# Performance work log

Measured on AMD Instinct MI355X. Metric: run time of the kernel, lower is better.

## Reference

```python
import jax, jax.numpy as jnp
import numpy as np

EPS = 1e-12
IMU_NOISE_DIAG = np.array([1e-07, 1e-07, 0.01, 0.001], dtype=np.float32)
INIT_COVAR_SQRT = np.array([0, 0, 0, 0, 0, 0, 0.01, 0.01, 0.01, 1e-4, 1e-4, 1e-4,
                            1e-08, 1e-08, 1e-08, 0.1, 0.1, 0.1], dtype=np.float32)
TRANS_SCALE = 5.4
TS2 = TRANS_SCALE * TRANS_SCALE
VIS_INIT_GUESS = 10.0 / TS2
VIS_BETA, VIS_GAMMA = 3.0, 1.0
IMU_BETA, IMU_GAMMA = 4.0, 1.0


def skew3(v):  # (..., 3) -> (..., 3, 3)
    x, y, z = v[..., 0], v[..., 1], v[..., 2]
    o = jnp.zeros_like(x)
    return jnp.stack([jnp.stack([o, -z, y], -1),
                      jnp.stack([z, o, -x], -1),
                      jnp.stack([-y, x, o], -1)], -2)


def exp_SO3(phi):  # (..., 3) -> (..., 3, 3) Rodrigues
    theta2 = jnp.sum(phi * phi, axis=-1)
    theta = jnp.sqrt(theta2)
    small = theta < 1e-8
    th = jnp.where(small, 1.0, theta)
    A = jnp.where(small, 1.0 - theta2 / 6.0, jnp.sin(th) / th)[..., None, None]
    B = jnp.where(small, 0.5 - theta2 / 24.0, (1.0 - jnp.cos(th)) / (th * th))[..., None, None]
    K = skew3(phi)
    return jnp.eye(3, dtype=phi.dtype) + A * K + B * (K @ K)


def force_symmetrical(M):
    Mu = jnp.triu(M)
    n = M.shape[-1]
    return Mu + jnp.swapaxes(Mu, -1, -2) * (1.0 - jnp.eye(n, dtype=M.dtype))


def proc_vis_covar(vis_std):
    # vis_covar_scale is all ones (par.vis_covar_scale = 1.0)
    scale = jnp.ones((6,), dtype=vis_std.dtype)
    diag = VIS_INIT_GUESS * (10.0 ** (VIS_BETA * jnp.tanh(VIS_GAMMA * vis_std)))
    diag = diag / scale[None, :]
    return jax.vmap(jnp.diag)(diag)  # (2B, 6, 6)


def get_imu_noise_covar(imu_noise_weight):
    # Linear(1,4,bias=False) applied to ones(1): just the weight column
    covar = 10.0 ** (IMU_BETA * jnp.tanh(IMU_GAMMA * imu_noise_weight[:, 0]))  # (4,)
    diag = jnp.repeat(jnp.asarray(IMU_NOISE_DIAG), 3) * jnp.repeat(covar, 3)   # (12,)
    return jnp.diag(diag)


def propagate(dts, wa_xyzs, R_ckbts, g_k, imu_noise_covar, P0):
    B = dts.shape[0]
    T = dts.shape[1]
    I3 = jnp.eye(3, dtype=dts.dtype)
    I18 = jnp.eye(18, dtype=dts.dtype)

    def step(P, inp):
        dt, gyro, accel, R = inp  # (B,), (B,3), (B,3), (B,3,3)
        Rt = jnp.swapaxes(R, -1, -2)
        w = gyro  # bw_k = 0
        Rg = jnp.einsum('bij,bj->bi', Rt, g_k)
        a = accel - Rg  # ba_k = 0
        F = jnp.zeros((B, 18, 18), dtype=dt.dtype)
        F = F.at[:, 0:3, 0:3].set(-skew3(w))
        F = F.at[:, 0:3, 12:15].set(-I3)
        F = F.at[:, 3:6, 6:9].set(I3)
        F = F.at[:, 6:9, 0:3].set(-jnp.einsum('bij,bjk->bik', R, skew3(Rg + a)))
        F = F.at[:, 6:9, 9:12].set(-I3)
        F = F.at[:, 6:9, 15:18].set(-R)
        G = jnp.zeros((B, 18, 12), dtype=dt.dtype)
        G = G.at[:, 0:3, 0:3].set(-I3)
        G = G.at[:, 6:9, 6:9].set(-R)
        G = G.at[:, 12:15, 3:6].set(I3)
        G = G.at[:, 15:18, 9:12].set(I3)
        dtb = dt[:, None, None]
        Phi = I18 + F * dtb + 0.5 * (F @ F) * (dtb * dtb)
        Phi = Phi.at[:, 0:3, 0:3].set(jnp.swapaxes(exp_SO3(dt[:, None] * w), -1, -2))
        PhiT = jnp.swapaxes(Phi, -1, -2)
        Q = (Phi @ G @ imu_noise_covar @ jnp.swapaxes(G, -1, -2) @ PhiT) * dtb
        P = force_symmetrical(Phi @ P @ PhiT + Q)
        return P, None

    xs = (jnp.swapaxes(dts, 0, 1),                       # (T, B)
          jnp.swapaxes(wa_xyzs[:, :T, :3], 0, 1),        # (T, B, 3)
          jnp.swapaxes(wa_xyzs[:, :T, 3:], 0, 1),        # (T, B, 3)
          jnp.swapaxes(R_ckbts[:, :T], 0, 1))            # (T, B, 3, 3)
    P, _ = jax.lax.scan(step, P0, xs)
    return P


def update(preimu_rot, preimu_trans, P, vis_rot, vis_trans, vis_covar, H0, H1, v_ck, g_ck):
    B = vis_rot.shape[0]
    residual = jnp.concatenate([vis_rot - preimu_rot, vis_trans - preimu_trans], axis=1)  # (B,6)
    I3 = jnp.eye(3, dtype=vis_rot.dtype)
    H = jnp.zeros((B, 6, 18), dtype=vis_rot.dtype)
    H = H.at[:, 0:3, 0:3].set(H0)
    H = H.at[:, 3:6, 0:3].set(H1)
    H = H.at[:, 3:6, 3:6].set(I3)
    Ht = jnp.swapaxes(H, -1, -2)
    S = H @ P @ Ht + vis_covar                 # (B,6,6)
    K = P @ Ht @ jnp.linalg.inv(S)             # (B,18,6)
    est = K @ residual[..., None]              # (B,18,1)
    phi_e, p_e = est[:, 0:3], est[:, 3:6]
    v_e, g_e = est[:, 6:9], est[:, 9:12]
    ekf_phi = preimu_rot + (H0 @ phi_e)[..., 0]
    ekf_t = preimu_trans + (H1 @ phi_e)[..., 0] + p_e[..., 0]
    return ekf_phi, ekf_t, v_ck + v_e[..., 0], g_ck + g_e[..., 0]


def setup_inputs() -> dict:
    key = jax.random.key(0)
    ks = jax.random.split(key, 16)
    B2 = 8192
    d = {
        'dts': jax.random.uniform(ks[0], (B2, 11), jnp.float32) * 0.01,
        'wa_xyzs': jax.random.normal(ks[1], (B2, 12, 6), jnp.float32),
        'R_ckbts': jax.random.normal(ks[2], (B2, 12, 3, 3), jnp.float32),
        'velocities': jax.random.normal(ks[3], (B2, 3), jnp.float32),
        'gravities': jax.random.normal(ks[4], (B2, 3), jnp.float32),
        'H0': jax.random.normal(ks[5], (B2, 3, 3), jnp.float32),
        'H1': jax.random.normal(ks[6], (B2, 3, 3), jnp.float32),
        'preimu_rot': jax.random.normal(ks[7], (B2, 3), jnp.float32),
        'preimu_trans': jax.random.normal(ks[8], (B2, 3), jnp.float32),
        'vis_rot': jax.random.normal(ks[9], (B2, 3), jnp.float32),
        'vis_trans': jax.random.normal(ks[10], (B2, 3), jnp.float32),
        'vis_rot_std': jax.random.uniform(ks[11], (B2, 3), jnp.float32),
        'vis_trans_std': jax.random.uniform(ks[12], (B2, 3), jnp.float32),
        'init_covar_diag_sqrt': jnp.asarray(INIT_COVAR_SQRT),
        'imu_noise_weight': jnp.zeros((4, 1), jnp.float32),  # train_imu_noise_covar=False -> zeroed
    }
    return d


def reference(dts, wa_xyzs, R_ckbts, velocities, gravities, H0, H1,
              preimu_rot, preimu_trans, vis_rot, vis_trans,
              vis_rot_std, vis_trans_std, init_covar_diag_sqrt, imu_noise_weight):
    B2 = dts.shape[0]
    vis_std = jnp.concatenate([vis_rot_std, vis_trans_std], axis=1)
    vis_covar = proc_vis_covar(vis_std)
    vis_trans = vis_trans * TRANS_SCALE
    imu_noise_covar = get_imu_noise_covar(imu_noise_weight)
    P0_diag = init_covar_diag_sqrt * init_covar_diag_sqrt + EPS
    P0 = jnp.broadcast_to(jnp.diag(P0_diag), (B2, 18, 18))
    P = propagate(dts, wa_xyzs, R_ckbts, gravities, imu_noise_covar, P0)
    ekf_phi, ekf_t, ekf_v, ekf_g = update(preimu_rot, preimu_trans, P,
                                          vis_rot, vis_trans, vis_covar,
                                          H0, H1, velocities, gravities)
    return jnp.concatenate([ekf_phi, ekf_t, ekf_v, ekf_g], axis=1)  # (2B, 12)
```

## Files before the change

kernel.cpp:

```cpp
#include <hip/hip_runtime.h>
#include <math.h>

#define TSTEPS 11
#define PPB 7
#define LPP 9
#define STRIDE 228
#define PHT_OFF 0
#define S6_OFF 144
#define Y_OFF 192
#define EST_OFF 200

__device__ __forceinline__ float sel3(int c, float a, float b, float d) {
    float t = (c == 1) ? b : a;
    return (c == 2) ? d : t;
}

__global__ void __launch_bounds__(64)
ekf_kernel(const float* __restrict__ dts, const float* __restrict__ wa,
           const float* __restrict__ Rc, const float* __restrict__ vel,
           const float* __restrict__ grav, const float* __restrict__ H0g,
           const float* __restrict__ H1g, const float* __restrict__ prot,
           const float* __restrict__ ptrans, const float* __restrict__ vrot,
           const float* __restrict__ vtrans, const float* __restrict__ vrstd,
           const float* __restrict__ vtstd, const float* __restrict__ icds,
           const float* __restrict__ inw, float* __restrict__ out, int B)
{
    __shared__ __align__(16) float lds[PPB * STRIDE];
    const int tid = threadIdx.x;
    const int praw = tid / LPP;
    const int r = tid - praw * LPP;
    const int p = (praw < PPB) ? praw : (PPB - 1);
    const int b0 = blockIdx.x * PPB + p;
    const bool valid = (praw < PPB) && (b0 < B);
    const int b = (b0 < B) ? b0 : (B - 1);
    float* L = lds + p * STRIDE;

    const float qcA = 1e-7f * exp10f(4.f * tanhf(inw[0]));
    const float qcB = 1e-7f * exp10f(4.f * tanhf(inw[1]));
    const float qcC = 1e-2f * exp10f(4.f * tanhf(inw[2]));
    const float qcD = 1e-3f * exp10f(4.f * tanhf(inw[3]));

    const float g0 = grav[(size_t)b*3+0], g1 = grav[(size_t)b*3+1], g2 = grav[(size_t)b*3+2];

    float np[18], npb[18];
#pragma unroll
    for (int k = 0; k < 18; ++k) { np[k] = 0.f; npb[k] = 0.f; }
    { const float d0 = icds[r];     np[r]      = d0*d0 + 1e-12f;
      const float d1 = icds[9 + r]; npb[9 + r] = d1*d1 + 1e-12f; }

    float dt, Rm[9], w0, w1, w2, ar0, ar1, ar2;
    {
        dt = dts[(size_t)b * TSTEPS];
        const size_t rb = (size_t)b * 108;
#pragma unroll
        for (int i = 0; i < 9; ++i) Rm[i] = Rc[rb + i];
        const float2* wp = (const float2*)(wa + (size_t)b * 72);
        const float2 wq0 = wp[0], wq1 = wp[1], wq2 = wp[2];
        w0 = wq0.x; w1 = wq0.y; w2 = wq1.x; ar0 = wq1.y; ar1 = wq2.x; ar2 = wq2.y;
    }

    for (int t = 0; t < TSTEPS; ++t) {
        float dtn = 0.f, Rn[9], wn0 = 0.f, wn1 = 0.f, wn2 = 0.f, an0 = 0.f, an1 = 0.f, an2 = 0.f;
#pragma unroll
        for (int i = 0; i < 9; ++i) Rn[i] = 0.f;
        if (t + 1 < TSTEPS) {
            dtn = dts[(size_t)b * TSTEPS + t + 1];
            const size_t rb = (size_t)b * 108 + (size_t)(t + 1) * 9;
#pragma unroll
            for (int i = 0; i < 9; ++i) Rn[i] = Rc[rb + i];
            const float2* wp = (const float2*)(wa + (size_t)b * 72 + (size_t)(t + 1) * 6);
            const float2 wq0 = wp[0], wq1 = wp[1], wq2 = wp[2];
            wn0 = wq0.x; wn1 = wq0.y; wn2 = wq1.x; an0 = wq1.y; an1 = wq2.x; an2 = wq2.y;
        }

        const float hdt2 = 0.5f * dt * dt;
        const float Rg0 = Rm[0]*g0 + Rm[3]*g1 + Rm[6]*g2;
        const float Rg1 = Rm[1]*g0 + Rm[4]*g1 + Rm[7]*g2;
        const float Rg2 = Rm[2]*g0 + Rm[5]*g1 + Rm[8]*g2;
        const float a0 = Rg0 + (ar0 - Rg0);
        const float a1 = Rg1 + (ar1 - Rg1);
        const float a2 = Rg2 + (ar2 - Rg2);

        const float p0 = dt*w0, p1 = dt*w1, p2 = dt*w2;
        const float th2 = p0*p0 + p1*p1 + p2*p2;
        const float th4 = th2 * th2;
        const float A  = 1.f - th2*(1.f/6.f)  + th4*(1.f/120.f);
        const float Bc = 0.5f - th2*(1.f/24.f) + th4*(1.f/720.f);
        float E[9];
        E[0] =  Bc*(p0*p0 - th2);  E[1] =  A*p2 + Bc*p0*p1;  E[2] = -A*p1 + Bc*p0*p2;
        E[3] = -A*p2 + Bc*p1*p0;   E[4] =  Bc*(p1*p1 - th2); E[5] =  A*p0 + Bc*p1*p2;
        E[6] =  A*p1 + Bc*p2*p0;   E[7] = -A*p0 + Bc*p2*p1;  E[8] =  Bc*(p2*p2 - th2);
        float N[9];
        N[0] = -(Rm[1]*a2 - Rm[2]*a1);  N[1] = -(Rm[2]*a0 - Rm[0]*a2);  N[2] = -(Rm[0]*a1 - Rm[1]*a0);
        N[3] = -(Rm[4]*a2 - Rm[5]*a1);  N[4] = -(Rm[5]*a0 - Rm[3]*a2);  N[5] = -(Rm[3]*a1 - Rm[4]*a0);
        N[6] = -(Rm[7]*a2 - Rm[8]*a1);  N[7] = -(Rm[8]*a0 - Rm[6]*a2);  N[8] = -(Rm[6]*a1 - Rm[7]*a0);
        float M2[9];
#pragma unroll
        for (int c = 0; c < 3; ++c) {
            const float n0 = N[c*3], n1 = N[c*3+1], n2 = N[c*3+2];
            M2[c*3+0] = dt*n0 - hdt2*(n1*w2 - n2*w1);
            M2[c*3+1] = dt*n1 - hdt2*(n2*w0 - n0*w2);
            M2[c*3+2] = dt*n2 - hdt2*(n0*w1 - n1*w0);
        }

        auto Smv = [&](const float v[18], float o[9]) {
            const float ev0 = E[0]*v[0] + E[1]*v[1] + E[2]*v[2];
            const float ev1 = E[3]*v[0] + E[4]*v[1] + E[5]*v[2];
            const float ev2 = E[6]*v[0] + E[7]*v[1] + E[8]*v[2];
            const float cx0 = w1*v[14] - w2*v[13];
            const float cx1 = w2*v[12] - w0*v[14];
            const float cx2 = w0*v[13] - w1*v[12];
            o[0] = ev0 - dt*v[12] + hdt2*cx0;
            o[1] = ev1 - dt*v[13] + hdt2*cx1;
            o[2] = ev2 - dt*v[14] + hdt2*cx2;
            const float nv0 = N[0]*v[0] + N[1]*v[1] + N[2]*v[2];
            const float nv1 = N[3]*v[0] + N[4]*v[1] + N[5]*v[2];
            const float nv2 = N[6]*v[0] + N[7]*v[1] + N[8]*v[2];
            const float rv0 = Rm[0]*v[15] + Rm[1]*v[16] + Rm[2]*v[17];
            const float rv1 = Rm[3]*v[15] + Rm[4]*v[16] + Rm[5]*v[17];
            const float rv2 = Rm[6]*v[15] + Rm[7]*v[16] + Rm[8]*v[17];
            o[3] = hdt2*nv0 + dt*v[6] - hdt2*v[9]  - hdt2*rv0;
            o[4] = hdt2*nv1 + dt*v[7] - hdt2*v[10] - hdt2*rv1;
            o[5] = hdt2*nv2 + dt*v[8] - hdt2*v[11] - hdt2*rv2;
            const float mv0 = M2[0]*v[0] + M2[1]*v[1] + M2[2]*v[2];
            const float mv1 = M2[3]*v[0] + M2[4]*v[1] + M2[5]*v[2];
            const float mv2 = M2[6]*v[0] + M2[7]*v[1] + M2[8]*v[2];
            const float nw0 = N[0]*v[12] + N[1]*v[13] + N[2]*v[14];
            const float nw1 = N[3]*v[12] + N[4]*v[13] + N[5]*v[14];
            const float nw2 = N[6]*v[12] + N[7]*v[13] + N[8]*v[14];
            o[6] = mv0 - dt*v[9]  - hdt2*nw0 - dt*rv0;
            o[7] = mv1 - dt*v[10] - hdt2*nw1 - dt*rv1;
            o[8] = mv2 - dt*v[11] - hdt2*nw2 - dt*rv2;
        };

        float uca[9], ucb[9];
        Smv(np, uca);
        Smv(npb, ucb);
#pragma unroll
        for (int i = 0; i < 9; ++i) {
            L[i*20 + r]     = uca[i];
            L[i*20 + 9 + r] = ucb[i];
        }
        __syncthreads();

        float ur[18];
        {
            const float4* up = (const float4*)&L[r*20];
            const float4 q0 = up[0], q1 = up[1], q2 = up[2], q3 = up[3];
            const float2 q4 = *(const float2*)&L[r*20 + 16];
            ur[0]=q0.x; ur[1]=q0.y; ur[2]=q0.z; ur[3]=q0.w;
            ur[4]=q1.x; ur[5]=q1.y; ur[6]=q1.z; ur[7]=q1.w;
            ur[8]=q2.x; ur[9]=q2.y; ur[10]=q2.z; ur[11]=q2.w;
            ur[12]=q3.x; ur[13]=q3.y; ur[14]=q3.z; ur[15]=q3.w;
            ur[16]=q4.x; ur[17]=q4.y;
        }

        float mr[12];
#pragma unroll
        for (int k = 0; k < 12; ++k) mr[k] = 0.f;
        if (r < 3) {
            mr[0] = -(((r==0)?1.f:0.f) + sel3(r, E[0], E[3], E[6]));
            mr[1] = -(((r==1)?1.f:0.f) + sel3(r, E[1], E[4], E[7]));
            mr[2] = -(((r==2)?1.f:0.f) + sel3(r, E[2], E[5], E[8]));
            mr[3] = ((r==0)?-dt:0.f) + hdt2*sel3(r, 0.f,  w2, -w1);
            mr[4] = ((r==1)?-dt:0.f) + hdt2*sel3(r, -w2, 0.f,  w0);
            mr[5] = ((r==2)?-dt:0.f) + hdt2*sel3(r,  w1, -w0, 0.f);
        } else if (r < 6) {
            const int c = r - 3;
            mr[0] = -hdt2*sel3(c, N[0], N[3], N[6]);
            mr[1] = -hdt2*sel3(c, N[1], N[4], N[7]);
            mr[2] = -hdt2*sel3(c, N[2], N[5], N[8]);
            mr[3] = (c==0)?-hdt2:0.f; mr[4] = (c==1)?-hdt2:0.f; mr[5] = (c==2)?-hdt2:0.f;
            const float q0 = sel3(c, Rm[0], Rm[3], Rm[6]);
            const float q1 = sel3(c, Rm[1], Rm[4], Rm[7]);
            const float q2 = sel3(c, Rm[2], Rm[5], Rm[8]);
            mr[6] = -dt*q0;   mr[7] = -dt*q1;   mr[8] = -dt*q2;
            mr[9] = -hdt2*q0; mr[10] = -hdt2*q1; mr[11] = -hdt2*q2;
        } else {
            const int c = r - 6;
            mr[0] = -sel3(c, M2[0], M2[3], M2[6]);
            mr[1] = -sel3(c, M2[1], M2[4], M2[7]);
            mr[2] = -sel3(c, M2[2], M2[5], M2[8]);
            mr[3] = -hdt2*sel3(c, N[0], N[3], N[6]);
            mr[4] = -hdt2*sel3(c, N[1], N[4], N[7]);
            mr[5] = -hdt2*sel3(c, N[2], N[5], N[8]);
            const float q0 = sel3(c, Rm[0], Rm[3], Rm[6]);
            const float q1 = sel3(c, Rm[1], Rm[4], Rm[7]);
            const float q2 = sel3(c, Rm[2], Rm[5], Rm[8]);
            mr[6] = -q0;    mr[7] = -q1;    mr[8] = -q2;
            mr[9] = -dt*q0; mr[10] = -dt*q1; mr[11] = -dt*q2;
        }
        float z[12];
        z[0]=mr[0]*qcA; z[1]=mr[1]*qcA; z[2]=mr[2]*qcA;
        z[3]=mr[3]*qcB; z[4]=mr[4]*qcB; z[5]=mr[5]*qcB;
        z[6]=mr[6]*qcC; z[7]=mr[7]*qcC; z[8]=mr[8]*qcC;
        z[9]=mr[9]*qcD; z[10]=mr[10]*qcD; z[11]=mr[11]*qcD;

        float Qc9[9];
        {
            const float ez0 = E[0]*z[0]+E[1]*z[1]+E[2]*z[2];
            const float ez1 = E[3]*z[0]+E[4]*z[1]+E[5]*z[2];
            const float ez2 = E[6]*z[0]+E[7]*z[1]+E[8]*z[2];
            const float cz0 = w1*z[5]-w2*z[4];
            const float cz1 = w2*z[3]-w0*z[5];
            const float cz2 = w0*z[4]-w1*z[3];
            Qc9[0] = -(z[0]+ez0) - dt*z[3] + hdt2*cz0;
            Qc9[1] = -(z[1]+ez1) - dt*z[4] + hdt2*cz1;
            Qc9[2] = -(z[2]+ez2) - dt*z[5] + hdt2*cz2;
            const float nz0 = N[0]*z[0]+N[1]*z[1]+N[2]*z[2];
            const float nz1 = N[3]*z[0]+N[4]*z[1]+N[5]*z[2];
            const float nz2 = N[6]*z[0]+N[7]*z[1]+N[8]*z[2];
            const float rz0 = Rm[0]*z[6]+Rm[1]*z[7]+Rm[2]*z[8];
            const float rz1 = Rm[3]*z[6]+Rm[4]*z[7]+Rm[5]*z[8];
            const float rz2 = Rm[6]*z[6]+Rm[7]*z[7]+Rm[8]*z[8];
            const float sz0 = Rm[0]*z[9]+Rm[1]*z[10]+Rm[2]*z[11];
            const float sz1 = Rm[3]*z[9]+Rm[4]*z[10]+Rm[5]*z[11];
            const float sz2 = Rm[6]*z[9]+Rm[7]*z[10]+Rm[8]*z[11];
            Qc9[3] = -hdt2*nz0 - hdt2*z[3] - dt*rz0 - hdt2*sz0;
            Qc9[4] = -hdt2*nz1 - hdt2*z[4] - dt*rz1 - hdt2*sz1;
            Qc9[5] = -hdt2*nz2 - hdt2*z[5] - dt*rz2 - hdt2*sz2;
            const float mz0 = M2[0]*z[0]+M2[1]*z[1]+M2[2]*z[2];
            const float mz1 = M2[3]*z[0]+M2[4]*z[1]+M2[5]*z[2];
            const float mz2 = M2[6]*z[0]+M2[7]*z[1]+M2[8]*z[2];
            const float nu0 = N[0]*z[3]+N[1]*z[4]+N[2]*z[5];
            const float nu1 = N[3]*z[3]+N[4]*z[4]+N[5]*z[5];
            const float nu2 = N[6]*z[3]+N[7]*z[4]+N[8]*z[5];
            Qc9[6] = -mz0 - hdt2*nu0 - rz0 - dt*sz0;
            Qc9[7] = -mz1 - hdt2*nu1 - rz1 - dt*sz1;
            Qc9[8] = -mz2 - hdt2*nu2 - rz2 - dt*sz2;
        }

        float w9[9];
        Smv(ur, w9);

#pragma unroll
        for (int i = 0; i < 9; ++i)
            np[i] = np[i] + uca[i] + ur[i] + w9[i] + dt*Qc9[i];
        np[9]  += ur[9];              np[10] += ur[10];             np[11] += ur[11];
        np[12] += ur[12] + dt*z[3];   np[13] += ur[13] + dt*z[4];   np[14] += ur[14] + dt*z[5];
        np[15] += ur[15] + dt*z[9];   np[16] += ur[16] + dt*z[10];  np[17] += ur[17] + dt*z[11];

#pragma unroll
        for (int i = 0; i < 9; ++i) npb[i] += ucb[i];
        if (r >= 3 && r < 6) {
            const int c = r - 3;
            const float f = dt * qcB;
            const float kc0 = sel3(c, 0.f, -w2,  w1);
            const float kc1 = sel3(c,  w2, 0.f, -w0);
            const float kc2 = sel3(c, -w1,  w0, 0.f);
            npb[0] += f * (((c==0)?-dt:0.f) + hdt2*kc0);
            npb[1] += f * (((c==1)?-dt:0.f) + hdt2*kc1);
            npb[2] += f * (((c==2)?-dt:0.f) + hdt2*kc2);
            npb[3] += (c==0) ? -f*hdt2 : 0.f;
            npb[4] += (c==1) ? -f*hdt2 : 0.f;
            npb[5] += (c==2) ? -f*hdt2 : 0.f;
            npb[6] += -f*hdt2*sel3(c, N[0], N[1], N[2]);
            npb[7] += -f*hdt2*sel3(c, N[3], N[4], N[5]);
            npb[8] += -f*hdt2*sel3(c, N[6], N[7], N[8]);
        } else if (r >= 6) {
            const int c = r - 6;
            const float f = dt * qcD;
            const float rc0 = sel3(c, Rm[0], Rm[1], Rm[2]);
            const float rc1 = sel3(c, Rm[3], Rm[4], Rm[5]);
            const float rc2 = sel3(c, Rm[6], Rm[7], Rm[8]);
            npb[3] += -f*hdt2*rc0;  npb[4] += -f*hdt2*rc1;  npb[5] += -f*hdt2*rc2;
            npb[6] += -f*dt*rc0;    npb[7] += -f*dt*rc1;    npb[8] += -f*dt*rc2;
        }
        npb[12] += (r==3) ? dt*qcB : 0.f;
        npb[13] += (r==4) ? dt*qcB : 0.f;
        npb[14] += (r==5) ? dt*qcB : 0.f;
        npb[15] += (r==6) ? dt*qcD : 0.f;
        npb[16] += (r==7) ? dt*qcD : 0.f;
        npb[17] += (r==8) ? dt*qcD : 0.f;

        __syncthreads();

        dt = dtn;
#pragma unroll
        for (int i = 0; i < 9; ++i) Rm[i] = Rn[i];
        w0 = wn0; w1 = wn1; w2 = wn2; ar0 = an0; ar1 = an1; ar2 = an2;
    }

    float h0v[9], h1v[9];
#pragma unroll
    for (int i = 0; i < 9; ++i) { h0v[i] = H0g[(size_t)b*9 + i]; h1v[i] = H1g[(size_t)b*9 + i]; }

    float phtA[6], phtB[6];
#pragma unroll
    for (int m = 0; m < 3; ++m) {
        phtA[m] = np[0]*h0v[m*3] + np[1]*h0v[m*3+1] + np[2]*h0v[m*3+2];
        phtB[m] = npb[0]*h0v[m*3] + npb[1]*h0v[m*3+1] + npb[2]*h0v[m*3+2];
    }
#pragma unroll
    for (int m = 3; m < 6; ++m) {
        phtA[m] = np[0]*h1v[(m-3)*3] + np[1]*h1v[(m-3)*3+1] + np[2]*h1v[(m-3)*3+2] + np[m];
        phtB[m] = npb[0]*h1v[(m-3)*3] + npb[1]*h1v[(m-3)*3+1] + npb[2]*h1v[(m-3)*3+2] + npb[m];
    }
#pragma unroll
    for (int m = 0; m < 6; ++m) {
        L[PHT_OFF + r*8 + m]       = phtA[m];
        L[PHT_OFF + (9 + r)*8 + m] = phtB[m];
    }
    __syncthreads();

    if (valid && r < 6) {
        const float* hp = (r < 3) ? (H0g + (size_t)b*9 + r*3)
                                  : (H1g + (size_t)b*9 + (r-3)*3);
        const float hr0 = hp[0], hr1 = hp[1], hr2 = hp[2];
        const float VIG = (float)(10.0 / (5.4 * 5.4));
#pragma unroll
        for (int n = 0; n < 6; ++n) {
            float v = hr0 * L[PHT_OFF + 0*8 + n] + hr1 * L[PHT_OFF + 1*8 + n]
                    + hr2 * L[PHT_OFF + 2*8 + n];
            if (r >= 3) v += phtA[n];
            if (n == r) {
                const float sd = (r < 3) ? vrstd[(size_t)b*3 + r] : vtstd[(size_t)b*3 + (r-3)];
                v += VIG * exp10f(3.f * tanhf(sd));
            }
            L[S6_OFF + r*8 + n] = v;
        }
        const float rs = (r < 3) ? (vrot[(size_t)b*3 + r] - prot[(size_t)b*3 + r])
                                 : (vtrans[(size_t)b*3 + (r-3)] * 5.4f - ptrans[(size_t)b*3 + (r-3)]);
        L[S6_OFF + r*8 + 6] = rs;
    }
    __syncthreads();

    if (valid && r == 0) {
        float a[6][7];
        const float* Sb = &L[S6_OFF];
#pragma unroll
        for (int m = 0; m < 6; ++m) {
            const float4 q0 = *(const float4*)&Sb[m*8];
            const float4 q1 = *(const float4*)&Sb[m*8 + 4];
            a[m][0]=q0.x; a[m][1]=q0.y; a[m][2]=q0.z; a[m][3]=q0.w;
            a[m][4]=q1.x; a[m][5]=q1.y; a[m][6]=q1.z;
        }
#pragma unroll
        for (int k = 0; k < 6; ++k) {
#pragma unroll
            for (int j = k + 1; j < 6; ++j) {
                const bool c = fabsf(a[j][k]) > fabsf(a[k][k]);
#pragma unroll
                for (int cc = k; cc < 7; ++cc) {
                    const float hi = c ? a[j][cc] : a[k][cc];
                    const float lo = c ? a[k][cc] : a[j][cc];
                    a[k][cc] = hi; a[j][cc] = lo;
                }
            }
            const float inv = 1.f / a[k][k];
#pragma unroll
            for (int j = 0; j < 6; ++j) {
                if (j == k) continue;
                const float f = a[j][k] * inv;
#pragma unroll
                for (int cc = k + 1; cc < 7; ++cc) a[j][cc] -= f * a[k][cc];
            }
        }
#pragma unroll
        for (int m = 0; m < 6; ++m) L[Y_OFF + m] = a[m][6] / a[m][m];
    }
    __syncthreads();

    float ym[6];
#pragma unroll
    for (int m = 0; m < 6; ++m) ym[m] = L[Y_OFF + m];
    float estr = 0.f, est9 = 0.f;
#pragma unroll
    for (int m = 0; m < 6; ++m) { estr += phtA[m]*ym[m]; est9 += phtB[m]*ym[m]; }
    if (valid) {
        L[EST_OFF + r] = estr;
        if (r < 3) L[EST_OFF + 9 + r] = est9;
    }
    __syncthreads();

    const float e0 = L[EST_OFF + 0], e1 = L[EST_OFF + 1], e2 = L[EST_OFF + 2];
    if (valid) {
        float o;
        if (r < 3) {
            const float* hq = H0g + (size_t)b*9 + r*3;
            o = prot[(size_t)b*3 + r] + hq[0]*e0 + hq[1]*e1 + hq[2]*e2;
        } else if (r < 6) {
            const int c = r - 3;
            const float* hq = H1g + (size_t)b*9 + c*3;
            o = ptrans[(size_t)b*3 + c] + hq[0]*e0 + hq[1]*e1 + hq[2]*e2 + estr;
        } else {
            o = vel[(size_t)b*3 + (r-6)] + estr;
        }
        out[(size_t)b*12 + r] = o;
        if (r < 3) out[(size_t)b*12 + 9 + r] = grav[(size_t)b*3 + r] + est9;
    }
}

extern "C" void kernel_launch(void* const* d_in, const int* in_sizes, int n_in,
                              void* d_out, int out_size, void* d_ws, size_t ws_size,
                              hipStream_t stream) {
    const float* dts    = (const float*)d_in[0];
    const float* wa     = (const float*)d_in[1];
    const float* Rc     = (const float*)d_in[2];
    const float* vel    = (const float*)d_in[3];
    const float* grav   = (const float*)d_in[4];
    const float* H0g    = (const float*)d_in[5];
    const float* H1g    = (const float*)d_in[6];
    const float* prot   = (const float*)d_in[7];
    const float* ptrans = (const float*)d_in[8];
    const float* vrot   = (const float*)d_in[9];
    const float* vtrans = (const float*)d_in[10];
    const float* vrstd  = (const float*)d_in[11];
    const float* vtstd  = (const float*)d_in[12];
    const float* icds   = (const float*)d_in[13];
    const float* inw    = (const float*)d_in[14];
    float* outp = (float*)d_out;

    const int B = in_sizes[0] / TSTEPS;
    const int grid = (B + PPB - 1) / PPB;
    hipLaunchKernelGGL(ekf_kernel, dim3(grid), dim3(64), 0, stream,
                       dts, wa, Rc, vel, grav, H0g, H1g, prot, ptrans,
                       vrot, vtrans, vrstd, vtstd, icds, inw, outp, B);
}
```

Baseline: 39.65 us.

## Split covariance rows across 18 lanes per problem instead of 9

Each problem now gets 18 threads, one per covariance row, instead of 9 threads that each carried two rows (np and npb). Problems per 64-thread block drop from 7 to 3. Lanes 0-8 run the full row update and lanes 9-17 run the simpler lower-row update, which halves per-thread registers and work but makes the two lane groups diverge within a wave. The change also needs more blocks and uses 54 of 64 lanes instead of 63.

```diff
diff --git a/kernel.cpp b/kernel.cpp
--- a/kernel.cpp
+++ b/kernel.cpp
@@ -2,8 +2,8 @@
 #include <math.h>
 
 #define TSTEPS 11
-#define PPB 7
-#define LPP 9
+#define PPB 3
+#define LPP 18
 #define STRIDE 228
 #define PHT_OFF 0
 #define S6_OFF 144
@@ -42,11 +42,10 @@
 
     const float g0 = grav[(size_t)b*3+0], g1 = grav[(size_t)b*3+1], g2 = grav[(size_t)b*3+2];
 
-    float np[18], npb[18];
-#pragma unroll
-    for (int k = 0; k < 18; ++k) { np[k] = 0.f; npb[k] = 0.f; }
-    { const float d0 = icds[r];     np[r]      = d0*d0 + 1e-12f;
-      const float d1 = icds[9 + r]; npb[9 + r] = d1*d1 + 1e-12f; }
+    float np[18];
+#pragma unroll
+    for (int k = 0; k < 18; ++k) np[k] = 0.f;
+    { const float d0 = icds[r]; np[r] = d0*d0 + 1e-12f; }
 
     float dt, Rm[9], w0, w1, w2, ar0, ar1, ar2;
     {
@@ -133,145 +132,139 @@
             o[8] = mv2 - dt*v[11] - hdt2*nw2 - dt*rv2;
         };
 
-        float uca[9], ucb[9];
+        float uca[9];
         Smv(np, uca);
-        Smv(npb, ucb);
-#pragma unroll
-        for (int i = 0; i < 9; ++i) {
-            L[i*20 + r]     = uca[i];
-            L[i*20 + 9 + r] = ucb[i];
-        }
+#pragma unroll
+        for (int i = 0; i < 9; ++i) L[i*20 + r] = uca[i];
         __syncthreads();
 
-        float ur[18];
-        {
-            const float4* up = (const float4*)&L[r*20];
-            const float4 q0 = up[0], q1 = up[1], q2 = up[2], q3 = up[3];
-            const float2 q4 = *(const float2*)&L[r*20 + 16];
-            ur[0]=q0.x; ur[1]=q0.y; ur[2]=q0.z; ur[3]=q0.w;
-            ur[4]=q1.x; ur[5]=q1.y; ur[6]=q1.z; ur[7]=q1.w;
-            ur[8]=q2.x; ur[9]=q2.y; ur[10]=q2.z; ur[11]=q2.w;
-            ur[12]=q3.x; ur[13]=q3.y; ur[14]=q3.z; ur[15]=q3.w;
-            ur[16]=q4.x; ur[17]=q4.y;
-        }
-
-        float mr[12];
-#pragma unroll
-        for (int k = 0; k < 12; ++k) mr[k] = 0.f;
-        if (r < 3) {
-            mr[0] = -(((r==0)?1.f:0.f) + sel3(r, E[0], E[3], E[6]));
-            mr[1] = -(((r==1)?1.f:0.f) + sel3(r, E[1], E[4], E[7]));
-            mr[2] = -(((r==2)?1.f:0.f) + sel3(r, E[2], E[5], E[8]));
-            mr[3] = ((r==0)?-dt:0.f) + hdt2*sel3(r, 0.f,  w2, -w1);
-            mr[4] = ((r==1)?-dt:0.f) + hdt2*sel3(r, -w2, 0.f,  w0);
-            mr[5] = ((r==2)?-dt:0.f) + hdt2*sel3(r,  w1, -w0, 0.f);
-        } else if (r < 6) {
-            const int c = r - 3;
-            mr[0] = -hdt2*sel3(c, N[0], N[3], N[6]);
-            mr[1] = -hdt2*sel3(c, N[1], N[4], N[7]);
-            mr[2] = -hdt2*sel3(c, N[2], N[5], N[8]);
-            mr[3] = (c==0)?-hdt2:0.f; mr[4] = (c==1)?-hdt2:0.f; mr[5] = (c==2)?-hdt2:0.f;
-            const float q0 = sel3(c, Rm[0], Rm[3], Rm[6]);
-            const float q1 = sel3(c, Rm[1], Rm[4], Rm[7]);
-            const float q2 = sel3(c, Rm[2], Rm[5], Rm[8]);
-            mr[6] = -dt*q0;   mr[7] = -dt*q1;   mr[8] = -dt*q2;
-            mr[9] = -hdt2*q0; mr[10] = -hdt2*q1; mr[11] = -hdt2*q2;
+        if (r < 9) {
+            float ur[18];
+            {
+                const float4* up = (const float4*)&L[r*20];
+                const float4 q0 = up[0], q1 = up[1], q2 = up[2], q3 = up[3];
+                const float2 q4 = *(const float2*)&L[r*20 + 16];
+                ur[0]=q0.x; ur[1]=q0.y; ur[2]=q0.z; ur[3]=q0.w;
+                ur[4]=q1.x; ur[5]=q1.y; ur[6]=q1.z; ur[7]=q1.w;
+                ur[8]=q2.x; ur[9]=q2.y; ur[10]=q2.z; ur[11]=q2.w;
+                ur[12]=q3.x; ur[13]=q3.y; ur[14]=q3.z; ur[15]=q3.w;
+                ur[16]=q4.x; ur[17]=q4.y;
+            }
+
+            float mr[12];
+#pragma unroll
+            for (int k = 0; k < 12; ++k) mr[k] = 0.f;
+            if (r < 3) {
+                mr[0] = -(((r==0)?1.f:0.f) + sel3(r, E[0], E[3], E[6]));
+                mr[1] = -(((r==1)?1.f:0.f) + sel3(r, E[1], E[4], E[7]));
+                mr[2] = -(((r==2)?1.f:0.f) + sel3(r, E[2], E[5], E[8]));
+                mr[3] = ((r==0)?-dt:0.f) + hdt2*sel3(r, 0.f,  w2, -w1);
+                mr[4] = ((r==1)?-dt:0.f) + hdt2*sel3(r, -w2, 0.f,  w0);
+                mr[5] = ((r==2)?-dt:0.f) + hdt2*sel3(r,  w1, -w0, 0.f);
+            } else if (r < 6) {
+                const int c = r - 3;
+                mr[0] = -hdt2*sel3(c, N[0], N[3], N[6]);
+                mr[1] = -hdt2*sel3(c, N[1], N[4], N[7]);
+                mr[2] = -hdt2*sel3(c, N[2], N[5], N[8]);
+                mr[3] = (c==0)?-hdt2:0.f; mr[4] = (c==1)?-hdt2:0.f; mr[5] = (c==2)?-hdt2:0.f;
+                const float q0 = sel3(c, Rm[0], Rm[3], Rm[6]);
+                const float q1 = sel3(c, Rm[1], Rm[4], Rm[7]);
+                const float q2 = sel3(c, Rm[2], Rm[5], Rm[8]);
+                mr[6] = -dt*q0;   mr[7] = -dt*q1;   mr[8] = -dt*q2;
+                mr[9] = -hdt2*q0; mr[10] = -hdt2*q1; mr[11] = -hdt2*q2;
+            } else {
+                const int c = r - 6;
+                mr[0] = -sel3(c, M2[0], M2[3], M2[6]);
+                mr[1] = -sel3(c, M2[1], M2[4], M2[7]);
+                mr[2] = -sel3(c, M2[2], M2[5], M2[8]);
+                mr[3] = -hdt2*sel3(c, N[0], N[3], N[6]);
+                mr[4] = -hdt2*sel3(c, N[1], N[4], N[7]);
+                mr[5] = -hdt2*sel3(c, N[2], N[5], N[8]);
+                const float q0 = sel3(c, Rm[0], Rm[3], Rm[6]);
+                const float q1 = sel3(c, Rm[1], Rm[4], Rm[7]);
+                const float q2 = sel3(c, Rm[2], Rm[5], Rm[8]);
+                mr[6] = -q0;    mr[7] = -q1;    mr[8] = -q2;
+                mr[9] = -dt*q0; mr[10] = -dt*q1; mr[11] = -dt*q2;
+            }
+            float z[12];
+            z[0]=mr[0]*qcA; z[1]=mr[1]*qcA; z[2]=mr[2]*qcA;
+            z[3]=mr[3]*qcB; z[4]=mr[4]*qcB; z[5]=mr[5]*qcB;
+            z[6]=mr[6]*qcC; z[7]=mr[7]*qcC; z[8]=mr[8]*qcC;
+            z[9]=mr[9]*qcD; z[10]=mr[10]*qcD; z[11]=mr[11]*qcD;
+
+            float Qc9[9];
+            {
+                const float ez0 = E[0]*z[0]+E[1]*z[1]+E[2]*z[2];
+                const float ez1 = E[3]*z[0]+E[4]*z[1]+E[5]*z[2];
+                const float ez2 = E[6]*z[0]+E[7]*z[1]+E[8]*z[2];
+                const float cz0 = w1*z[5]-w2*z[4];
+                const float cz1 = w2*z[3]-w0*z[5];
+                const float cz2 = w0*z[4]-w1*z[3];
+                Qc9[0] = -(z[0]+ez0) - dt*z[3] + hdt2*cz0;
+                Qc9[1] = -(z[1]+ez1) - dt*z[4] + hdt2*cz1;
+                Qc9[2] = -(z[2]+ez2) - dt*z[5] + hdt2*cz2;
+                const float nz0 = N[0]*z[0]+N[1]*z[1]+N[2]*z[2];
+                const float nz1 = N[3]*z[0]+N[4]*z[1]+N[5]*z[2];
+                const float nz2 = N[6]*z[0]+N[7]*z[1]+N[8]*z[2];
+                const float rz0 = Rm[0]*z[6]+Rm[1]*z[7]+Rm[2]*z[8];
+                const float rz1 = Rm[3]*z[6]+Rm[4]*z[7]+Rm[5]*z[8];
+                const float rz2 = Rm[6]*z[6]+Rm[7]*z[7]+Rm[8]*z[8];
+                const float sz0 = Rm[0]*z[9]+Rm[1]*z[10]+Rm[2]*z[11];
+                const float sz1 = Rm[3]*z[9]+Rm[4]*z[10]+Rm[5]*z[11];
+                const float sz2 = Rm[6]*z[9]+Rm[7]*z[10]+Rm[8]*z[11];
+                Qc9[3] = -hdt2*nz0 - hdt2*z[3] - dt*rz0 - hdt2*sz0;
+                Qc9[4] = -hdt2*nz1 - hdt2*z[4] - dt*rz1 - hdt2*sz1;
+                Qc9[5] = -hdt2*nz2 - hdt2*z[5] - dt*rz2 - hdt2*sz2;
+                const float mz0 = M2[0]*z[0]+M2[1]*z[1]+M2[2]*z[2];
+                const float mz1 = M2[3]*z[0]+M2[4]*z[1]+M2[5]*z[2];
+                const float mz2 = M2[6]*z[0]+M2[7]*z[1]+M2[8]*z[2];
+                const float nu0 = N[0]*z[3]+N[1]*z[4]+N[2]*z[5];
+                const float nu1 = N[3]*z[3]+N[4]*z[4]+N[5]*z[5];
+                const float nu2 = N[6]*z[3]+N[7]*z[4]+N[8]*z[5];
+                Qc9[6] = -mz0 - hdt2*nu0 - rz0 - dt*sz0;
+                Qc9[7] = -mz1 - hdt2*nu1 - rz1 - dt*sz1;
+                Qc9[8] = -mz2 - hdt2*nu2 - rz2 - dt*sz2;
+            }
+
+            float w9[9];
+            Smv(ur, w9);
+
+#pragma unroll
+            for (int i = 0; i < 9; ++i)
+                np[i] = np[i] + uca[i] + ur[i] + w9[i] + dt*Qc9[i];
+            np[9]  += ur[9];              np[10] += ur[10];             np[11] += ur[11];
+            np[12] += ur[12] + dt*z[3];   np[13] += ur[13] + dt*z[4];   np[14] += ur[14] + dt*z[5];
+            np[15] += ur[15] + dt*z[9];   np[16] += ur[16] + dt*z[10];  np[17] += ur[17] + dt*z[11];
         } else {
-            const int c = r - 6;
-            mr[0] = -sel3(c, M2[0], M2[3], M2[6]);
-            mr[1] = -sel3(c, M2[1], M2[4], M2[7]);
-            mr[2] = -sel3(c, M2[2], M2[5], M2[8]);
-            mr[3] = -hdt2*sel3(c, N[0], N[3], N[6]);
-            mr[4] = -hdt2*sel3(c, N[1], N[4], N[7]);
-            mr[5] = -hdt2*sel3(c, N[2], N[5], N[8]);
-            const float q0 = sel3(c, Rm[0], Rm[3], Rm[6]);
-            const float q1 = sel3(c, Rm[1], Rm[4], Rm[7]);
-            const float q2 = sel3(c, Rm[2], Rm[5], Rm[8]);
-            mr[6] = -q0;    mr[7] = -q1;    mr[8] = -q2;
-            mr[9] = -dt*q0; mr[10] = -dt*q1; mr[11] = -dt*q2;
-        }
-        float z[12];
-        z[0]=mr[0]*qcA; z[1]=mr[1]*qcA; z[2]=mr[2]*qcA;
-        z[3]=mr[3]*qcB; z[4]=mr[4]*qcB; z[5]=mr[5]*qcB;
-        z[6]=mr[6]*qcC; z[7]=mr[7]*qcC; z[8]=mr[8]*qcC;
-        z[9]=mr[9]*qcD; z[10]=mr[10]*qcD; z[11]=mr[11]*qcD;
-
-        float Qc9[9];
-        {
-            const float ez0 = E[0]*z[0]+E[1]*z[1]+E[2]*z[2];
-            const float ez1 = E[3]*z[0]+E[4]*z[1]+E[5]*z[2];
-            const float ez2 = E[6]*z[0]+E[7]*z[1]+E[8]*z[2];
-            const float cz0 = w1*z[5]-w2*z[4];
-            const float cz1 = w2*z[3]-w0*z[5];
-            const float cz2 = w0*z[4]-w1*z[3];
-            Qc9[0] = -(z[0]+ez0) - dt*z[3] + hdt2*cz0;
-            Qc9[1] = -(z[1]+ez1) - dt*z[4] + hdt2*cz1;
-            Qc9[2] = -(z[2]+ez2) - dt*z[5] + hdt2*cz2;
-            const float nz0 = N[0]*z[0]+N[1]*z[1]+N[2]*z[2];
-            const float nz1 = N[3]*z[0]+N[4]*z[1]+N[5]*z[2];
-            const float nz2 = N[6]*z[0]+N[7]*z[1]+N[8]*z[2];
-            const float rz0 = Rm[0]*z[6]+Rm[1]*z[7]+Rm[2]*z[8];
-            const float rz1 = Rm[3]*z[6]+Rm[4]*z[7]+Rm[5]*z[8];
-            const float rz2 = Rm[6]*z[6]+Rm[7]*z[7]+Rm[8]*z[8];
-            const float sz0 = Rm[0]*z[9]+Rm[1]*z[10]+Rm[2]*z[11];
-            const float sz1 = Rm[3]*z[9]+Rm[4]*z[10]+Rm[5]*z[11];
-            const float sz2 = Rm[6]*z[9]+Rm[7]*z[10]+Rm[8]*z[11];
-            Qc9[3] = -hdt2*nz0 - hdt2*z[3] - dt*rz0 - hdt2*sz0;
-            Qc9[4] = -hdt2*nz1 - hdt2*z[4] - dt*rz1 - hdt2*sz1;
-            Qc9[5] = -hdt2*nz2 - hdt2*z[5] - dt*rz2 - hdt2*sz2;
-            const float mz0 = M2[0]*z[0]+M2[1]*z[1]+M2[2]*z[2];
-            const float mz1 = M2[3]*z[0]+M2[4]*z[1]+M2[5]*z[2];
-            const float mz2 = M2[6]*z[0]+M2[7]*z[1]+M2[8]*z[2];
-            const float nu0 = N[0]*z[3]+N[1]*z[4]+N[2]*z[5];
-            const float nu1 = N[3]*z[3]+N[4]*z[4]+N[5]*z[5];
-            const float nu2 = N[6]*z[3]+N[7]*z[4]+N[8]*z[5];
-            Qc9[6] = -mz0 - hdt2*nu0 - rz0 - dt*sz0;
-            Qc9[7] = -mz1 - hdt2*nu1 - rz1 - dt*sz1;
-            Qc9[8] = -mz2 - hdt2*nu2 - rz2 - dt*sz2;
-        }
-
-        float w9[9];
-        Smv(ur, w9);
-
-#pragma unroll
-        for (int i = 0; i < 9; ++i)
-            np[i] = np[i] + uca[i] + ur[i] + w9[i] + dt*Qc9[i];
-        np[9]  += ur[9];              np[10] += ur[10];             np[11] += ur[11];
-        np[12] += ur[12] + dt*z[3];   np[13] += ur[13] + dt*z[4];   np[14] += ur[14] + dt*z[5];
-        np[15] += ur[15] + dt*z[9];   np[16] += ur[16] + dt*z[10];  np[17] += ur[17] + dt*z[11];
-
-#pragma unroll
-        for (int i = 0; i < 9; ++i) npb[i] += ucb[i];
-        if (r >= 3 && r < 6) {
-            const int c = r - 3;
-            const float f = dt * qcB;
-            const float kc0 = sel3(c, 0.f, -w2,  w1);
-            const float kc1 = sel3(c,  w2, 0.f, -w0);
-            const float kc2 = sel3(c, -w1,  w0, 0.f);
-            npb[0] += f * (((c==0)?-dt:0.f) + hdt2*kc0);
-            npb[1] += f * (((c==1)?-dt:0.f) + hdt2*kc1);
-            npb[2] += f * (((c==2)?-dt:0.f) + hdt2*kc2);
-            npb[3] += (c==0) ? -f*hdt2 : 0.f;
-            npb[4] += (c==1) ? -f*hdt2 : 0.f;
-            npb[5] += (c==2) ? -f*hdt2 : 0.f;
-            npb[6] += -f*hdt2*sel3(c, N[0], N[1], N[2]);
-            npb[7] += -f*hdt2*sel3(c, N[3], N[4], N[5]);
-            npb[8] += -f*hdt2*sel3(c, N[6], N[7], N[8]);
-        } else if (r >= 6) {
-            const int c = r - 6;
-            const float f = dt * qcD;
-            const float rc0 = sel3(c, Rm[0], Rm[1], Rm[2]);
-            const float rc1 = sel3(c, Rm[3], Rm[4], Rm[5]);
-            const float rc2 = sel3(c, Rm[6], Rm[7], Rm[8]);
-            npb[3] += -f*hdt2*rc0;  npb[4] += -f*hdt2*rc1;  npb[5] += -f*hdt2*rc2;
-            npb[6] += -f*dt*rc0;    npb[7] += -f*dt*rc1;    npb[8] += -f*dt*rc2;
-        }
-        npb[12] += (r==3) ? dt*qcB : 0.f;
-        npb[13] += (r==4) ? dt*qcB : 0.f;
-        npb[14] += (r==5) ? dt*qcB : 0.f;
-        npb[15] += (r==6) ? dt*qcD : 0.f;
-        npb[16] += (r==7) ? dt*qcD : 0.f;
-        npb[17] += (r==8) ? dt*qcD : 0.f;
+#pragma unroll
+            for (int i = 0; i < 9; ++i) np[i] += uca[i];
+            const int rr = r - 9;
+            if (rr >= 3 && rr < 6) {
+                const int c = rr - 3;
+                const float f = dt * qcB;
+                const float kc0 = sel3(c, 0.f, -w2,  w1);
+                const float kc1 = sel3(c,  w2, 0.f, -w0);
+                const float kc2 = sel3(c, -w1,  w0, 0.f);
+                np[0] += f * (((c==0)?-dt:0.f) + hdt2*kc0);
+                np[1] += f * (((c==1)?-dt:0.f) + hdt2*kc1);
+                np[2] += f * (((c==2)?-dt:0.f) + hdt2*kc2);
+                np[3] += (c==0) ? -f*hdt2 : 0.f;
+                np[4] += (c==1) ? -f*hdt2 : 0.f;
+                np[5] += (c==2) ? -f*hdt2 : 0.f;
+                np[6] += -f*hdt2*sel3(c, N[0], N[1], N[2]);
+                np[7] += -f*hdt2*sel3(c, N[3], N[4], N[5]);
+                np[8] += -f*hdt2*sel3(c, N[6], N[7], N[8]);
+            } else if (rr >= 6) {
+                const int c = rr - 6;
+                const float f = dt * qcD;
+                const float rc0 = sel3(c, Rm[0], Rm[1], Rm[2]);
+                const float rc1 = sel3(c, Rm[3], Rm[4], Rm[5]);
+                const float rc2 = sel3(c, Rm[6], Rm[7], Rm[8]);
+                np[3] += -f*hdt2*rc0;  np[4] += -f*hdt2*rc1;  np[5] += -f*hdt2*rc2;
+                np[6] += -f*dt*rc0;    np[7] += -f*dt*rc1;    np[8] += -f*dt*rc2;
+            }
+            if (r >= 12) np[r] += dt * ((r < 15) ? qcB : qcD);
+        }
 
         __syncthreads();
 
@@ -285,22 +278,15 @@
 #pragma unroll
     for (int i = 0; i < 9; ++i) { h0v[i] = H0g[(size_t)b*9 + i]; h1v[i] = H1g[(size_t)b*9 + i]; }
 
-    float phtA[6], phtB[6];
-#pragma unroll
-    for (int m = 0; m < 3; ++m) {
+    float phtA[6];
+#pragma unroll
+    for (int m = 0; m < 3; ++m)
         phtA[m] = np[0]*h0v[m*3] + np[1]*h0v[m*3+1] + np[2]*h0v[m*3+2];
-        phtB[m] = npb[0]*h0v[m*3] + npb[1]*h0v[m*3+1] + npb[2]*h0v[m*3+2];
-    }
-#pragma unroll
-    for (int m = 3; m < 6; ++m) {
+#pragma unroll
+    for (int m = 3; m < 6; ++m)
         phtA[m] = np[0]*h1v[(m-3)*3] + np[1]*h1v[(m-3)*3+1] + np[2]*h1v[(m-3)*3+2] + np[m];
-        phtB[m] = npb[0]*h1v[(m-3)*3] + npb[1]*h1v[(m-3)*3+1] + npb[2]*h1v[(m-3)*3+2] + npb[m];
-    }
-#pragma unroll
-    for (int m = 0; m < 6; ++m) {
-        L[PHT_OFF + r*8 + m]       = phtA[m];
-        L[PHT_OFF + (9 + r)*8 + m] = phtB[m];
-    }
+#pragma unroll
+    for (int m = 0; m < 6; ++m) L[PHT_OFF + r*8 + m] = phtA[m];
     __syncthreads();
 
     if (valid && r < 6) {
@@ -364,17 +350,14 @@
     float ym[6];
 #pragma unroll
     for (int m = 0; m < 6; ++m) ym[m] = L[Y_OFF + m];
-    float estr = 0.f, est9 = 0.f;
-#pragma unroll
-    for (int m = 0; m < 6; ++m) { estr += phtA[m]*ym[m]; est9 += phtB[m]*ym[m]; }
-    if (valid) {
-        L[EST_OFF + r] = estr;
-        if (r < 3) L[EST_OFF + 9 + r] = est9;
-    }
+    float estr = 0.f;
+#pragma unroll
+    for (int m = 0; m < 6; ++m) estr += phtA[m]*ym[m];
+    if (valid && r < 3) L[EST_OFF + r] = estr;
     __syncthreads();
 
     const float e0 = L[EST_OFF + 0], e1 = L[EST_OFF + 1], e2 = L[EST_OFF + 2];
-    if (valid) {
+    if (valid && r < 12) {
         float o;
         if (r < 3) {
             const float* hq = H0g + (size_t)b*9 + r*3;
@@ -383,11 +366,12 @@
             const int c = r - 3;
             const float* hq = H1g + (size_t)b*9 + c*3;
             o = ptrans[(size_t)b*3 + c] + hq[0]*e0 + hq[1]*e1 + hq[2]*e2 + estr;
+        } else if (r < 9) {
+            o = vel[(size_t)b*3 + (r-6)] + estr;
         } else {
-            o = vel[(size_t)b*3 + (r-6)] + estr;
+            o = grav[(size_t)b*3 + (r-9)] + estr;
         }
         out[(size_t)b*12 + r] = o;
-        if (r < 3) out[(size_t)b*12 + 9 + r] = grav[(size_t)b*3 + r] + est9;
     }
 }
 
```

New measurement: 52.70 us. 32.9% more time.

## Stage per-step IMU inputs in LDS with coalesced loads and hoist epilogue loads

Applied to the files above, without the earlier changes.

Before the time loop, the whole block loads all 11 steps of dts, gyro/accel and rotation matrices for its batch elements into shared memory, using coalesced float4 reads. This replaces the per-thread, per-step prefetch of strided global data. The H, visual std, residual and velocity loads are also hoisted to the kernel start so their latency overlaps the propagation. The cost is extra LDS use per block, one added barrier, and more live registers across the loop.

```diff
diff --git a/kernel.cpp b/kernel.cpp
--- a/kernel.cpp
+++ b/kernel.cpp
@@ -4,7 +4,8 @@
 #define TSTEPS 11
 #define PPB 7
 #define LPP 9
-#define STRIDE 228
+#define IN_STRIDE 192
+#define WSTRIDE 228
 #define PHT_OFF 0
 #define S6_OFF 144
 #define Y_OFF 192
@@ -14,6 +15,8 @@
     float t = (c == 1) ? b : a;
     return (c == 2) ? d : t;
 }
+
+__device__ __forceinline__ size_t umin_sz(size_t a, size_t b) { return a < b ? a : b; }
 
 __global__ void __launch_bounds__(64)
 ekf_kernel(const float* __restrict__ dts, const float* __restrict__ wa,
@@ -25,15 +28,50 @@
            const float* __restrict__ vtstd, const float* __restrict__ icds,
            const float* __restrict__ inw, float* __restrict__ out, int B)
 {
-    __shared__ __align__(16) float lds[PPB * STRIDE];
+    __shared__ __align__(16) float gin[PPB * IN_STRIDE];
+    __shared__ __align__(16) float lds[PPB * WSTRIDE];
     const int tid = threadIdx.x;
     const int praw = tid / LPP;
     const int r = tid - praw * LPP;
     const int p = (praw < PPB) ? praw : (PPB - 1);
-    const int b0 = blockIdx.x * PPB + p;
+    const int blk0 = blockIdx.x * PPB;
+    const int b0 = blk0 + p;
     const bool valid = (praw < PPB) && (b0 < B);
     const int b = (b0 < B) ? b0 : (B - 1);
-    float* L = lds + p * STRIDE;
+    float* L = lds + p * WSTRIDE;
+    const float* gi = gin + p * IN_STRIDE;
+
+    {
+        const size_t dmax = (size_t)B * 11 - 1;
+        for (int e = tid; e < PPB * 11; e += 64) {
+            const int pp = e / 11, o = e - pp * 11;
+            gin[pp * IN_STRIDE + o] = dts[umin_sz((size_t)blk0 * 11 + e, dmax)];
+        }
+        const size_t wmax4 = (size_t)B * 18 - 1;
+        const float4* wa4 = (const float4*)wa;
+        for (int e = tid; e < PPB * 18; e += 64) {
+            const int pp = e / 18, o = e - pp * 18;
+            *(float4*)&gin[pp * IN_STRIDE + 12 + o * 4] = wa4[umin_sz((size_t)blk0 * 18 + e, wmax4)];
+        }
+        const size_t rmax4 = (size_t)B * 27 - 1;
+        const float4* Rc4 = (const float4*)Rc;
+        for (int e = tid; e < PPB * 27; e += 64) {
+            const int pp = e / 27, o = e - pp * 27;
+            *(float4*)&gin[pp * IN_STRIDE + 84 + o * 4] = Rc4[umin_sz((size_t)blk0 * 27 + e, rmax4)];
+        }
+    }
+
+    float h0v[9], h1v[9];
+#pragma unroll
+    for (int i = 0; i < 9; ++i) { h0v[i] = H0g[(size_t)b * 9 + i]; h1v[i] = H1g[(size_t)b * 9 + i]; }
+    const int rc6 = (r < 6) ? r : 5;
+    const float* hpr = (rc6 < 3) ? (H0g + (size_t)b * 9 + rc6 * 3)
+                                 : (H1g + (size_t)b * 9 + (rc6 - 3) * 3);
+    const float hr0 = hpr[0], hr1 = hpr[1], hr2 = hpr[2];
+    const float sdv = (rc6 < 3) ? vrstd[(size_t)b * 3 + rc6] : vtstd[(size_t)b * 3 + (rc6 - 3)];
+    const float rsa = (rc6 < 3) ? vrot[(size_t)b * 3 + rc6] : vtrans[(size_t)b * 3 + (rc6 - 3)];
+    const float rsb = (rc6 < 3) ? prot[(size_t)b * 3 + rc6] : ptrans[(size_t)b * 3 + (rc6 - 3)];
+    const float velv = vel[(size_t)b * 3 + ((r >= 6) ? (r - 6) : 0)];
 
     const float qcA = 1e-7f * exp10f(4.f * tanhf(inw[0]));
     const float qcB = 1e-7f * exp10f(4.f * tanhf(inw[1]));
@@ -48,30 +86,18 @@
     { const float d0 = icds[r];     np[r]      = d0*d0 + 1e-12f;
       const float d1 = icds[9 + r]; npb[9 + r] = d1*d1 + 1e-12f; }
 
-    float dt, Rm[9], w0, w1, w2, ar0, ar1, ar2;
-    {
-        dt = dts[(size_t)b * TSTEPS];
-        const size_t rb = (size_t)b * 108;
-#pragma unroll
-        for (int i = 0; i < 9; ++i) Rm[i] = Rc[rb + i];
-        const float2* wp = (const float2*)(wa + (size_t)b * 72);
-        const float2 wq0 = wp[0], wq1 = wp[1], wq2 = wp[2];
-        w0 = wq0.x; w1 = wq0.y; w2 = wq1.x; ar0 = wq1.y; ar1 = wq2.x; ar2 = wq2.y;
-    }
+    __syncthreads();
 
     for (int t = 0; t < TSTEPS; ++t) {
-        float dtn = 0.f, Rn[9], wn0 = 0.f, wn1 = 0.f, wn2 = 0.f, an0 = 0.f, an1 = 0.f, an2 = 0.f;
-#pragma unroll
-        for (int i = 0; i < 9; ++i) Rn[i] = 0.f;
-        if (t + 1 < TSTEPS) {
-            dtn = dts[(size_t)b * TSTEPS + t + 1];
-            const size_t rb = (size_t)b * 108 + (size_t)(t + 1) * 9;
-#pragma unroll
-            for (int i = 0; i < 9; ++i) Rn[i] = Rc[rb + i];
-            const float2* wp = (const float2*)(wa + (size_t)b * 72 + (size_t)(t + 1) * 6);
-            const float2 wq0 = wp[0], wq1 = wp[1], wq2 = wp[2];
-            wn0 = wq0.x; wn1 = wq0.y; wn2 = wq1.x; an0 = wq1.y; an1 = wq2.x; an2 = wq2.y;
-        }
+        const float dt = gi[t];
+        const float2 wq0 = *(const float2*)&gi[12 + t * 6];
+        const float2 wq1 = *(const float2*)&gi[12 + t * 6 + 2];
+        const float2 wq2 = *(const float2*)&gi[12 + t * 6 + 4];
+        const float w0 = wq0.x, w1 = wq0.y, w2 = wq1.x;
+        const float ar0 = wq1.y, ar1 = wq2.x, ar2 = wq2.y;
+        float Rm[9];
+#pragma unroll
+        for (int i = 0; i < 9; ++i) Rm[i] = gi[84 + t * 9 + i];
 
         const float hdt2 = 0.5f * dt * dt;
         const float Rg0 = Rm[0]*g0 + Rm[3]*g1 + Rm[6]*g2;
@@ -274,16 +300,7 @@
         npb[17] += (r==8) ? dt*qcD : 0.f;
 
         __syncthreads();
-
-        dt = dtn;
-#pragma unroll
-        for (int i = 0; i < 9; ++i) Rm[i] = Rn[i];
-        w0 = wn0; w1 = wn1; w2 = wn2; ar0 = an0; ar1 = an1; ar2 = an2;
-    }
-
-    float h0v[9], h1v[9];
-#pragma unroll
-    for (int i = 0; i < 9; ++i) { h0v[i] = H0g[(size_t)b*9 + i]; h1v[i] = H1g[(size_t)b*9 + i]; }
+    }
 
     float phtA[6], phtB[6];
 #pragma unroll
@@ -304,24 +321,16 @@
     __syncthreads();
 
     if (valid && r < 6) {
-        const float* hp = (r < 3) ? (H0g + (size_t)b*9 + r*3)
-                                  : (H1g + (size_t)b*9 + (r-3)*3);
-        const float hr0 = hp[0], hr1 = hp[1], hr2 = hp[2];
         const float VIG = (float)(10.0 / (5.4 * 5.4));
 #pragma unroll
         for (int n = 0; n < 6; ++n) {
             float v = hr0 * L[PHT_OFF + 0*8 + n] + hr1 * L[PHT_OFF + 1*8 + n]
                     + hr2 * L[PHT_OFF + 2*8 + n];
             if (r >= 3) v += phtA[n];
-            if (n == r) {
-                const float sd = (r < 3) ? vrstd[(size_t)b*3 + r] : vtstd[(size_t)b*3 + (r-3)];
-                v += VIG * exp10f(3.f * tanhf(sd));
-            }
+            if (n == r) v += VIG * exp10f(3.f * tanhf(sdv));
             L[S6_OFF + r*8 + n] = v;
         }
-        const float rs = (r < 3) ? (vrot[(size_t)b*3 + r] - prot[(size_t)b*3 + r])
-                                 : (vtrans[(size_t)b*3 + (r-3)] * 5.4f - ptrans[(size_t)b*3 + (r-3)]);
-        L[S6_OFF + r*8 + 6] = rs;
+        L[S6_OFF + r*8 + 6] = (r < 3) ? (rsa - rsb) : (rsa * 5.4f - rsb);
     }
     __syncthreads();
 
@@ -377,17 +386,14 @@
     if (valid) {
         float o;
         if (r < 3) {
-            const float* hq = H0g + (size_t)b*9 + r*3;
-            o = prot[(size_t)b*3 + r] + hq[0]*e0 + hq[1]*e1 + hq[2]*e2;
+            o = rsb + hr0*e0 + hr1*e1 + hr2*e2;
         } else if (r < 6) {
-            const int c = r - 3;
-            const float* hq = H1g + (size_t)b*9 + c*3;
-            o = ptrans[(size_t)b*3 + c] + hq[0]*e0 + hq[1]*e1 + hq[2]*e2 + estr;
+            o = rsb + hr0*e0 + hr1*e1 + hr2*e2 + estr;
         } else {
-            o = vel[(size_t)b*3 + (r-6)] + estr;
+            o = velv + estr;
         }
         out[(size_t)b*12 + r] = o;
-        if (r < 3) out[(size_t)b*12 + 9 + r] = grav[(size_t)b*3 + r] + est9;
+        if (r < 3) out[(size_t)b*12 + 9 + r] = ((r==0)?g0:((r==1)?g1:g2)) + est9;
     }
 }
 
```

Result: faster. 37.76 us (-4.8%).
